# Optimization experiments

Hardware: AMD Instinct MI355X
Metric: run time of the kernel (lower is better)

## Reference

```python
import jax, jax.numpy as jnp
import numpy as np

H_OUT = 7
W_OUT = 7
SCALE = 1.0 / 16.0


def setup_inputs() -> dict:
    key = jax.random.key(0)
    k1, k2, k3, k4 = jax.random.split(key, 4)
    N, C, h, w = 2, 512, 50, 50      # VGG16 conv5 features of an 800x800 image (stride 16)
    R = 128                          # rois per minibatch
    img = 800.0
    x = jax.random.normal(k1, (N, C, h, w), dtype=jnp.float32)
    batch = jax.random.randint(k2, (R,), 0, N).astype(jnp.float32)
    pt1 = jax.random.uniform(k3, (R, 2), minval=0.0, maxval=img - 32.0)   # (y1, x1)
    sz = jax.random.uniform(k4, (R, 2), minval=32.0, maxval=400.0)
    pt2 = jnp.minimum(pt1 + sz, img - 1.0)                                # (y2, x2)
    rois = jnp.concatenate(
        [batch[:, None], pt1[:, 0:1], pt1[:, 1:2], pt2[:, 0:1], pt2[:, 1:2]], axis=1
    )
    return {"x": x, "rois": rois}


def roi_pool(x, rois, H=H_OUT, W=W_OUT, scale=SCALE):
    # Faithful to the source: each ROI is zero-padded up to multiples of (H, W),
    # tiled into non-overlapping HxW windows, and the output is the elementwise
    # max across windows (padding zeros participate in the max).
    N, C, h, w = x.shape
    R = rois.shape[0]
    bidx = rois[:, 0].astype(jnp.int32)
    bb = jnp.round(rois[:, 1:5] * scale).astype(jnp.int32)   # (y1, x1, y2, x2)
    y1, x1 = bb[:, 0], bb[:, 1]
    y2 = jnp.minimum(bb[:, 2], h - 1)   # torch slicing x[..., y1:y2+1] clips at h
    x2 = jnp.minimum(bb[:, 3], w - 1)

    ys = jnp.arange(h)
    xs = jnp.arange(w)
    in_y = (ys[None, :] >= y1[:, None]) & (ys[None, :] <= y2[:, None])   # [R, h]
    in_x = (xs[None, :] >= x1[:, None]) & (xs[None, :] <= x2[:, None])   # [R, w]
    a = jnp.mod(ys[None, :] - y1[:, None], H)   # within-window row   [R, h]
    b = jnp.mod(xs[None, :] - x1[:, None], W)   # within-window col   [R, w]

    valid = in_y[:, :, None] & in_x[:, None, :]                 # [R, h, w]
    bin_id = a[:, :, None] * W + b[:, None, :]                  # [R, h, w]
    roi_off = jnp.arange(R)[:, None, None] * (H * W)
    dump = R * H * W                                            # bin for pixels outside any ROI
    seg = jnp.where(valid, roi_off + bin_id, dump).reshape(-1)  # [R*h*w]

    vals = x[bidx]                                              # [R, C, h, w] gather per ROI
    vals = vals.transpose(0, 2, 3, 1).reshape(-1, C)            # [R*h*w, C]
    seg_max = jax.ops.segment_max(vals, seg, num_segments=R * H * W + 1)[: R * H * W]
    seg_max = seg_max.reshape(R, H, W, C).transpose(0, 3, 1, 2)  # [R, C, H, W]

    # Zero padding contributes to the max at bin (a, b) iff the ROI extent is not
    # an exact multiple of H (resp. W) and a >= ft_h % H (resp. b >= ft_w % W).
    ft_h = y2 - y1 + 1
    ft_w = x2 - x1 + 1
    rem_h = jnp.mod(ft_h, H)
    rem_w = jnp.mod(ft_w, W)
    pad_h = (rem_h[:, None] != 0) & (jnp.arange(H)[None, :] >= rem_h[:, None])  # [R, H]
    pad_w = (rem_w[:, None] != 0) & (jnp.arange(W)[None, :] >= rem_w[:, None])  # [R, W]
    zero_inc = pad_h[:, None, :, None] | pad_w[:, None, None, :]                # [R, 1, H, W]
    return jnp.where(zero_inc, jnp.maximum(seg_max, 0), seg_max).astype(x.dtype)


def reference(x, rois):
    return roi_pool(x, rois)
```

## Files before the change

kernel.cpp:

```cpp
#include <hip/hip_runtime.h>
#include <math.h>


#define CH 512
#define IH 50
#define IW 50
#define NEG_INF (-__builtin_inff())

__global__ __launch_bounds__(256) void roipool_kernel(
    const float* __restrict__ x, const float* __restrict__ rois,
    float* __restrict__ out) {
  const int r    = blockIdx.y;
  const int wave = threadIdx.x >> 6;
  const int lane = threadIdx.x & 63;
  const int half = lane >> 5;
  const int dx   = lane & 31;

  const float* rr = rois + r * 5;
  const int b  = __builtin_amdgcn_readfirstlane((int)rr[0]);
  const int y1 = __builtin_amdgcn_readfirstlane((int)rintf(rr[1] * 0.0625f));
  const int x1 = __builtin_amdgcn_readfirstlane((int)rintf(rr[2] * 0.0625f));
  const int y2 = __builtin_amdgcn_readfirstlane(min((int)rintf(rr[3] * 0.0625f), IH - 1));
  const int x2 = __builtin_amdgcn_readfirstlane(min((int)rintf(rr[4] * 0.0625f), IW - 1));
  const int fth  = y2 - y1 + 1;
  const int ftw  = x2 - x1 + 1;
  const int remh = fth % 7;
  const int remw = ftw % 7;
  const int full = fth / 7;

  const int cbase = (blockIdx.x * 4 + wave) * 4 + half * 2;
  const int cx    = min(dx, ftw - 1);
  const bool colok = dx < ftw;

  const float* b0 = x + ((size_t)(b * CH + cbase) * IH + y1) * IW + x1 + cx;
  const float* b1 = b0 + (size_t)IH * IW;

  float acc0[7], acc1[7];
#pragma unroll
  for (int i = 0; i < 7; ++i) { acc0[i] = NEG_INF; acc1[i] = NEG_INF; }

  for (int s = 0; s < full; ++s) {
    const float* r0 = b0 + s * 7 * IW;
    const float* r1 = b1 + s * 7 * IW;
#pragma unroll
    for (int i = 0; i < 7; ++i) {
      float v0 = r0[i * IW];
      float v1 = r1[i * IW];
      v0 = colok ? v0 : NEG_INF;
      v1 = colok ? v1 : NEG_INF;
      acc0[i] = fmaxf(acc0[i], v0);
      acc1[i] = fmaxf(acc1[i], v1);
    }
  }

  {
    const float* t0 = b0 + full * 7 * IW;
    const float* t1 = b1 + full * 7 * IW;
#pragma unroll
    for (int i = 0; i < 7; ++i) {
      if (i < remh) {
        float v0 = t0[i * IW];
        float v1 = t1[i * IW];
        v0 = colok ? v0 : NEG_INF;
        v1 = colok ? v1 : NEG_INF;
        acc0[i] = fmaxf(acc0[i], v0);
        acc1[i] = fmaxf(acc1[i], v1);
      }
    }
  }

#pragma unroll
  for (int i = 0; i < 7; ++i) {
    float a0 = acc0[i], a1 = acc1[i];
    a0 = fmaxf(a0, __shfl_down(a0, 7, 64));
    a1 = fmaxf(a1, __shfl_down(a1, 7, 64));
    a0 = fmaxf(a0, __shfl_down(a0, 14, 64));
    a1 = fmaxf(a1, __shfl_down(a1, 14, 64));
    acc0[i] = a0;
    acc1[i] = a1;
  }

  if (dx < 7) {
    const int j = dx;
    const bool padc = (remw != 0) && (j >= remw);
    float* o0 = out + (size_t)(r * CH + cbase) * 49 + j;
    float* o1 = o0 + 49;
#pragma unroll
    for (int i = 0; i < 7; ++i) {
      float v0 = acc0[i], v1 = acc1[i];
      const bool padr = (remh != 0) && (i >= remh);
      if (padr | padc) { v0 = fmaxf(v0, 0.0f); v1 = fmaxf(v1, 0.0f); }
      o0[i * 7] = v0;
      o1[i * 7] = v1;
    }
  }
}

extern "C" void kernel_launch(void* const* d_in, const int* in_sizes, int n_in,
                              void* d_out, int out_size, void* d_ws, size_t ws_size,
                              hipStream_t stream) {
  const float* x    = (const float*)d_in[0];
  const float* rois = (const float*)d_in[1];
  float* out        = (float*)d_out;
  const int R = in_sizes[1] / 5;

  dim3 grid(32, R);
  dim3 block(256);
  roipool_kernel<<<grid, block, 0, stream>>>(x, rois, out);
}
```

Before: 71.25 us.

## Remap lanes to 8 channels per wave with per-lane column strides, drop shuffles

```diff
diff --git a/kernel.cpp b/kernel.cpp
--- a/kernel.cpp
+++ b/kernel.cpp
@@ -7,14 +7,43 @@
 #define IW 50
 #define NEG_INF (-__builtin_inff())
 
+template <int NK>
+__device__ __forceinline__ void walk(const float* __restrict__ xp,
+                                     uint32_t (&voff)[4],
+                                     const bool (&colok)[4],
+                                     int full, int remh, float (&acc)[7]) {
+  for (int s = 0; s < full; ++s) {
+#pragma unroll
+    for (int i = 0; i < 7; ++i) {
+#pragma unroll
+      for (int k = 0; k < NK; ++k) {
+        float v = xp[voff[k] + (uint32_t)(i * IW)];
+        acc[i] = fmaxf(acc[i], colok[k] ? v : NEG_INF);
+      }
+    }
+#pragma unroll
+    for (int k = 0; k < NK; ++k) voff[k] += 7u * IW;
+  }
+#pragma unroll
+  for (int i = 0; i < 7; ++i) {
+    if (i < remh) {
+#pragma unroll
+      for (int k = 0; k < NK; ++k) {
+        float v = xp[voff[k] + (uint32_t)(i * IW)];
+        acc[i] = fmaxf(acc[i], colok[k] ? v : NEG_INF);
+      }
+    }
+  }
+}
+
 __global__ __launch_bounds__(256) void roipool_kernel(
     const float* __restrict__ x, const float* __restrict__ rois,
     float* __restrict__ out) {
   const int r    = blockIdx.y;
   const int wave = threadIdx.x >> 6;
   const int lane = threadIdx.x & 63;
-  const int half = lane >> 5;
-  const int dx   = lane & 31;
+  const int g    = lane >> 3;
+  const int j    = lane & 7;
 
   const float* rr = rois + r * 5;
   const int b  = __builtin_amdgcn_readfirstlane((int)rr[0]);
@@ -28,70 +57,40 @@
   const int remw = ftw % 7;
   const int full = fth / 7;
 
-  const int cbase = (blockIdx.x * 4 + wave) * 4 + half * 2;
-  const int cx    = min(dx, ftw - 1);
-  const bool colok = dx < ftw;
+  const int c = (blockIdx.x * 4 + wave) * 8 + g;
+  const uint32_t rowbase =
+      ((uint32_t)(b * CH + c) * IH + (uint32_t)y1) * IW + (uint32_t)x1;
 
-  const float* b0 = x + ((size_t)(b * CH + cbase) * IH + y1) * IW + x1 + cx;
-  const float* b1 = b0 + (size_t)IH * IW;
+  bool colok[4];
+  uint32_t voff[4];
+#pragma unroll
+  for (int k = 0; k < 4; ++k) {
+    const int col = j + 7 * k;
+    colok[k] = (j < 7) & (col < ftw);
+    voff[k]  = rowbase + (uint32_t)min(col, ftw - 1);
+  }
 
-  float acc0[7], acc1[7];
+  float acc[7];
 #pragma unroll
-  for (int i = 0; i < 7; ++i) { acc0[i] = NEG_INF; acc1[i] = NEG_INF; }
+  for (int i = 0; i < 7; ++i) acc[i] = NEG_INF;
 
-  for (int s = 0; s < full; ++s) {
-    const float* r0 = b0 + s * 7 * IW;
-    const float* r1 = b1 + s * 7 * IW;
+  const int nk = (ftw + 6) / 7;
+  switch (nk) {
+    case 1:  walk<1>(x, voff, colok, full, remh, acc); break;
+    case 2:  walk<2>(x, voff, colok, full, remh, acc); break;
+    case 3:  walk<3>(x, voff, colok, full, remh, acc); break;
+    default: walk<4>(x, voff, colok, full, remh, acc); break;
+  }
+
+  if (j < 7) {
+    const bool padc = (remw != 0) & (j >= remw);
+    float* o = out + (size_t)(r * CH + c) * 49 + j;
 #pragma unroll
     for (int i = 0; i < 7; ++i) {
-      float v0 = r0[i * IW];
-      float v1 = r1[i * IW];
-      v0 = colok ? v0 : NEG_INF;
-      v1 = colok ? v1 : NEG_INF;
-      acc0[i] = fmaxf(acc0[i], v0);
-      acc1[i] = fmaxf(acc1[i], v1);
-    }
-  }
-
-  {
-    const float* t0 = b0 + full * 7 * IW;
-    const float* t1 = b1 + full * 7 * IW;
-#pragma unroll
-    for (int i = 0; i < 7; ++i) {
-      if (i < remh) {
-        float v0 = t0[i * IW];
-        float v1 = t1[i * IW];
-        v0 = colok ? v0 : NEG_INF;
-        v1 = colok ? v1 : NEG_INF;
-        acc0[i] = fmaxf(acc0[i], v0);
-        acc1[i] = fmaxf(acc1[i], v1);
-      }
-    }
-  }
-
-#pragma unroll
-  for (int i = 0; i < 7; ++i) {
-    float a0 = acc0[i], a1 = acc1[i];
-    a0 = fmaxf(a0, __shfl_down(a0, 7, 64));
-    a1 = fmaxf(a1, __shfl_down(a1, 7, 64));
-    a0 = fmaxf(a0, __shfl_down(a0, 14, 64));
-    a1 = fmaxf(a1, __shfl_down(a1, 14, 64));
-    acc0[i] = a0;
-    acc1[i] = a1;
-  }
-
-  if (dx < 7) {
-    const int j = dx;
-    const bool padc = (remw != 0) && (j >= remw);
-    float* o0 = out + (size_t)(r * CH + cbase) * 49 + j;
-    float* o1 = o0 + 49;
-#pragma unroll
-    for (int i = 0; i < 7; ++i) {
-      float v0 = acc0[i], v1 = acc1[i];
-      const bool padr = (remh != 0) && (i >= remh);
-      if (padr | padc) { v0 = fmaxf(v0, 0.0f); v1 = fmaxf(v1, 0.0f); }
-      o0[i * 7] = v0;
-      o1[i * 7] = v1;
+      float v = acc[i];
+      const bool padr = (remh != 0) & (i >= remh);
+      if (padr | padc) v = fmaxf(v, 0.0f);
+      o[i * 7] = v;
     }
   }
 }
@@ -104,7 +103,7 @@
   float* out        = (float*)d_out;
   const int R = in_sizes[1] / 5;
 
-  dim3 grid(32, R);
+  dim3 grid(16, R);
   dim3 block(256);
   roipool_kernel<<<grid, block, 0, stream>>>(x, rois, out);
 }
```

Result: no change. 72.50 us (+1.8%).
